# Kernel tuning notes

Measured on AMD Instinct MI355X. Metric: run time of the kernel, lower is better.

The kernel has to match this reference:

```python
import jax, jax.numpy as jnp
import numpy as np

EPS = 1e-5   # torch BatchNorm2d default eps
HEADS = 4


def conv1x1_bn(x, w, g, b, m, v):
    # 1x1 conv (no bias) == channel matmul, then inference-mode BatchNorm
    y = jnp.einsum('oc,bchw->bohw', w, x)
    s = g / jnp.sqrt(v + EPS)
    return y * s[None, :, None, None] + (b - m * s)[None, :, None, None]


def dwconv3x3_bn(x, w, g, b, m, v):
    # depthwise 3x3 conv, padding 1 (autopad), groups=C, then BatchNorm
    C = x.shape[1]
    y = jax.lax.conv_general_dilated(
        x, w, window_strides=(1, 1), padding=((1, 1), (1, 1)),
        dimension_numbers=('NCHW', 'OIHW', 'NCHW'), feature_group_count=C)
    s = g / jnp.sqrt(v + EPS)
    return y * s[None, :, None, None] + (b - m * s)[None, :, None, None]


def split_heads(x):
    b, c, h, w = x.shape
    hd = c // HEADS
    return x.reshape(b, HEADS, hd, h * w).transpose(0, 1, 3, 2)  # [b,heads,n,hd]


def merge_heads(x, h, w):
    b, heads, n, hd = x.shape
    return x.transpose(0, 1, 3, 2).reshape(b, heads * hd, h, w)


def setup_inputs() -> dict:
    key = jax.random.key(0)
    B, C, H, W = 4, 256, 48, 48
    ks = jax.random.split(key, 32)
    inp = {
        'q': jax.random.normal(ks[0], (B, C, H, W), jnp.float32),
        'k': jax.random.normal(ks[1], (B, C, H, W), jnp.float32),
        'v': jax.random.normal(ks[2], (B, C, H, W), jnp.float32),
    }
    i = 3
    for name in ['wq', 'wk', 'wv', 'proj']:
        inp[name + '_w'] = jax.random.normal(ks[i], (C, C), jnp.float32) * 0.02; i += 1
    inp['pe_w'] = jax.random.normal(ks[i], (C, 1, 3, 3), jnp.float32) * 0.1; i += 1
    for name in ['wq', 'wk', 'wv', 'pe', 'proj']:
        inp[name + '_g'] = jax.random.uniform(ks[i], (C,), jnp.float32, 0.5, 1.5); i += 1
        inp[name + '_b'] = jax.random.normal(ks[i], (C,), jnp.float32) * 0.1; i += 1
        inp[name + '_m'] = jax.random.normal(ks[i], (C,), jnp.float32) * 0.1; i += 1
        inp[name + '_v'] = jax.random.uniform(ks[i], (C,), jnp.float32, 0.5, 1.5); i += 1
    return inp


def reference(q, k, v,
              wq_w, wk_w, wv_w, proj_w, pe_w,
              wq_g, wq_b, wq_m, wq_v,
              wk_g, wk_b, wk_m, wk_v,
              wv_g, wv_b, wv_m, wv_v,
              pe_g, pe_b, pe_m, pe_v,
              proj_g, proj_b, proj_m, proj_v):
    H, W = q.shape[2], q.shape[3]
    qf = conv1x1_bn(q, wq_w, wq_g, wq_b, wq_m, wq_v)
    kf = conv1x1_bn(k, wk_w, wk_g, wk_b, wk_m, wk_v)
    vf = conv1x1_bn(v, wv_w, wv_g, wv_b, wv_m, wv_v)
    qh = split_heads(qf)  # [b,heads,n,hd]
    kh = split_heads(kf)
    vh = split_heads(vf)
    scale = qh.shape[-1] ** -0.5
    attn = jax.nn.softmax(jnp.einsum('bhnd,bhmd->bhnm', qh, kh) * scale, axis=-1)
    y = jnp.einsum('bhnm,bhmd->bhnd', attn, vh)
    y = merge_heads(y, H, W) + dwconv3x3_bn(merge_heads(qh, H, W), pe_w, pe_g, pe_b, pe_m, pe_v)
    return conv1x1_bn(y, proj_w, proj_g, proj_b, proj_m, proj_v)
```

## Files before the change

### kernel.cpp

```cpp
#include <hip/hip_runtime.h>
#include <math.h>

#define HEADS 4
#define HD    64
#define CCH   256
#define NB    4
#define HH    48
#define WW    48
#define NN    (HH*WW)
#define EPSBN 1e-5f
#define KSCL  0.18033688f
#define BCN   (NB*CCH*NN)
#define NSP   4

typedef unsigned short ushort_t;
typedef __attribute__((ext_vector_type(8))) short bfrag;
typedef __attribute__((ext_vector_type(4))) float f32x4;
typedef __attribute__((ext_vector_type(16))) float f32x16;

#define MFMA   __builtin_amdgcn_mfma_f32_16x16x32_bf16
#define MFMA32 __builtin_amdgcn_mfma_f32_32x32x16_bf16

static __device__ __forceinline__ ushort_t f2bf(float x) {
    unsigned int u = __float_as_uint(x);
    unsigned int r = (u + 0x7fffu + ((u >> 16) & 1u)) >> 16;
    return (ushort_t)r;
}
static __device__ __forceinline__ unsigned cvtpk(float lo, float hi) {
    unsigned r;
    asm("v_cvt_pk_bf16_f32 %0, %1, %2" : "=v"(r) : "v"(lo), "v"(hi));
    return r;
}
static __device__ __forceinline__ float fexp2(float x) {
    float r;
    asm("v_exp_f32 %0, %1" : "=v"(r) : "v"(x));
    return r;
}
static __device__ __forceinline__ float bflo(unsigned u) { return __uint_as_float(u << 16); }
static __device__ __forceinline__ float bfhi(unsigned u) { return __uint_as_float(u & 0xffff0000u); }

static __device__ __forceinline__ void gload16(const void* g, void* l) {
    __builtin_amdgcn_global_load_lds(
        (const __attribute__((address_space(1))) void*)g,
        (__attribute__((address_space(3))) void*)l, 16, 0, 0);
}

struct PrepWP {
    const float* W[4];
    const float* G[4]; const float* Bb[4]; const float* Mm[4]; const float* Vv[4];
    const float* pew; const float* peg; const float* peb; const float* pem; const float* pev;
    ushort_t* W4; float* bias4; ushort_t* pw2; float* pbias;
};
__global__ __launch_bounds__(256)
void prep_w(PrepWP P)
{
    const int blk = blockIdx.x, tid = threadIdx.x;
    if (blk == 128) {
        int c = tid;
        float s = P.peg[c] * rsqrtf(P.pev[c] + EPSBN);
        for (int tap = 0; tap < 9; ++tap)
            P.pw2[tap * CCH + c] = f2bf(P.pew[c * 9 + tap] * s);
        P.pbias[c] = P.peb[c] - P.pem[c] * s;
        return;
    }
    int g  = blk * 256 + tid;
    int cv = g >> 13;
    int o  = (g >> 5) & 255;
    int c8 = g & 31;
    float s  = P.G[cv][o] * rsqrtf(P.Vv[cv][o] + EPSBN);
    float s2 = (cv == 1) ? s * KSCL : s;
    const float* w = P.W[cv] + (size_t)o * CCH + c8 * 8;
    uint4 u;
    u.x = cvtpk(w[0]*s2, w[1]*s2); u.y = cvtpk(w[2]*s2, w[3]*s2);
    u.z = cvtpk(w[4]*s2, w[5]*s2); u.w = cvtpk(w[6]*s2, w[7]*s2);
    *(uint4*)&P.W4[((size_t)cv * CCH + o) * CCH + c8 * 8] = u;
    if (c8 == 0) {
        float bb = (P.Bb[cv][o] - P.Mm[cv][o] * s);
        P.bias4[cv * CCH + o] = (cv == 1) ? bb * KSCL : bb;
    }
}

template<int PROJ>
__global__ __launch_bounds__(256)
void conv_gemm(const float* __restrict__ qf, const float* __restrict__ kf,
               const float* __restrict__ vf, const ushort_t* __restrict__ T,
               const ushort_t* __restrict__ W4, const float* __restrict__ bias4,
               ushort_t* __restrict__ qnd, ushort_t* __restrict__ knd,
               ushort_t* __restrict__ vcn, float* __restrict__ outf)
{
    __shared__ ushort_t Ts[64][264];
    __shared__ ushort_t Ws[64][264];
    const int nt = blockIdx.x, ot = blockIdx.y, z = blockIdx.z;
    const int which = PROJ ? 3 : (z >> 2);
    const int b = z & 3;
    const int tid = threadIdx.x;
    const int n0 = nt * 64, o0 = ot * 64;
    const ushort_t* Wsrc = W4 + (size_t)which * CCH * CCH + (size_t)o0 * CCH;
    const float*    bias = bias4 + which * CCH;

    if (!PROJ) {
#pragma unroll
        for (int i = 0; i < 8; ++i) {
            int idx = tid + i * 256;
            int r = idx >> 5, c16 = idx & 31;
            *(uint4*)&Ws[r][c16 * 8] = *(const uint4*)&Wsrc[(size_t)r * CCH + c16 * 8];
        }
        const float* Xf = (which == 0) ? qf : (which == 1) ? kf : vf;
        const float* Xb = Xf + (size_t)b * CCH * NN + n0;
        const int n = tid & 63;
#pragma unroll
        for (int p = 0; p < 8; ++p) {
            int c0 = (tid >> 6) * 8 + p * 32;
            const float* src = Xb + (size_t)c0 * NN + n;
            float vv[8];
#pragma unroll
            for (int j = 0; j < 8; ++j) vv[j] = src[(size_t)j * NN];
            uint4 u;
            u.x = cvtpk(vv[0], vv[1]); u.y = cvtpk(vv[2], vv[3]);
            u.z = cvtpk(vv[4], vv[5]); u.w = cvtpk(vv[6], vv[7]);
            *(uint4*)&Ts[n][c0] = u;
        }
    } else {
        const ushort_t* Tsrc = T + ((size_t)b * NN + n0) * CCH;
#pragma unroll
        for (int i = 0; i < 8; ++i) {
            int idx = tid + i * 256;
            int r = idx >> 5, c16 = idx & 31;
            *(uint4*)&Ts[r][c16 * 8] = *(const uint4*)&Tsrc[(size_t)r * CCH + c16 * 8];
            *(uint4*)&Ws[r][c16 * 8] = *(const uint4*)&Wsrc[(size_t)r * CCH + c16 * 8];
        }
    }
    __syncthreads();
    const int wv = tid >> 6, lane = tid & 63, lr = lane & 15, lg = lane >> 4;
    const int qn = (wv >> 1) * 32, qo = (wv & 1) * 32;
    f32x4 acc[2][2];
#pragma unroll
    for (int i = 0; i < 2; ++i)
#pragma unroll
        for (int j = 0; j < 2; ++j) acc[i][j] = (f32x4){0.f, 0.f, 0.f, 0.f};

    if (!PROJ && (z >> 2) < 2) {
#pragma unroll
        for (int k8 = 0; k8 < 8; ++k8) {
            const int kc = k8 * 32 + lg * 8;
            bfrag ta0 = *(const bfrag*)&Ts[qn + lr][kc];
            bfrag ta1 = *(const bfrag*)&Ts[qn + 16 + lr][kc];
            bfrag wa0 = *(const bfrag*)&Ws[qo + lr][kc];
            bfrag wa1 = *(const bfrag*)&Ws[qo + 16 + lr][kc];
            acc[0][0] = MFMA(ta0, wa0, acc[0][0], 0, 0, 0);
            acc[0][1] = MFMA(ta0, wa1, acc[0][1], 0, 0, 0);
            acc[1][0] = MFMA(ta1, wa0, acc[1][0], 0, 0, 0);
            acc[1][1] = MFMA(ta1, wa1, acc[1][1], 0, 0, 0);
        }
    } else {
#pragma unroll
        for (int k8 = 0; k8 < 8; ++k8) {
            const int kc = k8 * 32 + lg * 8;
            bfrag ta0 = *(const bfrag*)&Ts[qn + lr][kc];
            bfrag ta1 = *(const bfrag*)&Ts[qn + 16 + lr][kc];
            bfrag wa0 = *(const bfrag*)&Ws[qo + lr][kc];
            bfrag wa1 = *(const bfrag*)&Ws[qo + 16 + lr][kc];
            acc[0][0] = MFMA(wa0, ta0, acc[0][0], 0, 0, 0);
            acc[0][1] = MFMA(wa0, ta1, acc[0][1], 0, 0, 0);
            acc[1][0] = MFMA(wa1, ta0, acc[1][0], 0, 0, 0);
            acc[1][1] = MFMA(wa1, ta1, acc[1][1], 0, 0, 0);
        }
    }

    __syncthreads();
    if (!PROJ && which < 2) {
        ushort_t (*Ot)[72] = (ushort_t(*)[72])Ts;
        float bv[2] = { bias[o0 + qo + lr], bias[o0 + qo + 16 + lr] };
#pragma unroll
        for (int i = 0; i < 2; ++i)
#pragma unroll
            for (int j = 0; j < 2; ++j)
#pragma unroll
                for (int r = 0; r < 4; ++r)
                    Ot[qn + i * 16 + lg * 4 + r][qo + j * 16 + lr] = f2bf(acc[i][j][r] + bv[j]);
        __syncthreads();
        ushort_t* out = (which == 0) ? qnd : knd;
        for (int idx = tid; idx < 512; idx += 256) {
            int r = idx >> 3, sg = idx & 7;
            *(uint4*)&out[(((size_t)b * HEADS + ot) * NN + n0 + r) * HD + sg * 8] =
                *(const uint4*)&Ot[r][sg * 8];
        }
    } else if (!PROJ) {
        ushort_t (*Ot)[72] = (ushort_t(*)[72])Ts;
#pragma unroll
        for (int i = 0; i < 2; ++i)
#pragma unroll
            for (int r = 0; r < 4; ++r) {
                float bv = bias[o0 + qo + i * 16 + lg * 4 + r];
#pragma unroll
                for (int j = 0; j < 2; ++j)
                    Ot[qo + i * 16 + lg * 4 + r][qn + j * 16 + lr] = f2bf(acc[i][j][r] + bv);
            }
        __syncthreads();
        for (int idx = tid; idx < 512; idx += 256) {
            int r = idx >> 3, sg = idx & 7;
            *(uint4*)&vcn[((size_t)b * CCH + o0 + r) * NN + n0 + sg * 8] =
                *(const uint4*)&Ot[r][sg * 8];
        }
    } else {
        float (*Of)[68] = (float(*)[68])Ts;
#pragma unroll
        for (int i = 0; i < 2; ++i)
#pragma unroll
            for (int r = 0; r < 4; ++r) {
                float bv = bias[o0 + qo + i * 16 + lg * 4 + r];
#pragma unroll
                for (int j = 0; j < 2; ++j)
                    Of[qo + i * 16 + lg * 4 + r][qn + j * 16 + lr] = acc[i][j][r] + bv;
            }
        __syncthreads();
        for (int idx = tid; idx < 1024; idx += 256) {
            int r = idx >> 4, c4 = idx & 15;
            *(float4*)&outf[((size_t)b * CCH + o0 + r) * NN + n0 + c4 * 4] =
                *(const float4*)&Of[r][c4 * 4];
        }
    }
}

__global__ __launch_bounds__(256, 4)
void attn_kernel(const ushort_t* __restrict__ Qnd,
                 const ushort_t* __restrict__ Knd,
                 const ushort_t* __restrict__ Vcn,
                 ushort_t* __restrict__ Op,
                 float* __restrict__ Larr)
{
    __shared__ __align__(16) char smem[32768];

    const int tid = threadIdx.x;
    const int lin0 = blockIdx.x + 18 * blockIdx.y + 288 * blockIdx.z;
    const int w    = (lin0 & 7) * 144 + (lin0 >> 3);
    const int qt = w % 18;
    const int bh = (w / 18) & 15;
    const int sp = w / 288;
    const int b = bh >> 2, h = bh & 3;
    const int lane = tid & 63, wv = tid >> 6;
    const int l31 = lane & 31, hi = lane >> 5, l7 = lane & 7;
    const int lrow = lane >> 3, lslot = (lane & 7) ^ lrow;
    const int n0 = qt * 128;
    const size_t ndb = (size_t)(b * HEADS + h) * NN * HD;
    const size_t cnb = ((size_t)b * CCH + h * HD) * NN;

    const char* kgp = (const char*)(Knd + ndb) + (size_t)(sp * 576 + wv * 16 + lrow) * 128 + lslot * 16;
    const char* vgp = (const char*)(Vcn + cnb + sp * 576) + (size_t)(wv * 16 + lrow) * (NN * 2) + lslot * 16;
    char* kls = smem + wv * 2048;
    char* vls = smem + 16384 + wv * 2048;

#define STAGE(buf, t) do { \
    const char* kp_ = kgp + (size_t)(t) * 8192; \
    const char* vp_ = vgp + (size_t)(t) * 128; \
    char* kd_ = kls + (buf) * 8192; \
    char* vd_ = vls + (buf) * 8192; \
    gload16(kp_,              kd_); \
    gload16(kp_ + 1024,       kd_ + 1024); \
    gload16(vp_,              vd_); \
    gload16(vp_ + 8 * (NN*2), vd_ + 1024); \
} while (0)

    bfrag qb[4];
    {
        const ushort_t* qbase = Qnd + ndb + (size_t)(n0 + wv * 32 + l31) * HD + hi * 8;
#pragma unroll
        for (int ds = 0; ds < 4; ++ds)
            qb[ds] = *(const bfrag*)&qbase[ds * 16];
    }

    f32x16 o[2];
#pragma unroll
    for (int db = 0; db < 2; ++db)
#pragma unroll
        for (int j = 0; j < 16; ++j) o[db][j] = 0.f;
    float lacc0 = 0.f, lacc1 = 0.f;

    STAGE(0, 0);

    for (int t = 0; t < 9; ++t) {
        const int cur = t & 1;
        if (t < 8) {
            STAGE(cur ^ 1, t + 1);
            asm volatile("s_waitcnt vmcnt(4)" ::: "memory");
        } else {
            asm volatile("s_waitcnt vmcnt(0)" ::: "memory");
        }
        __builtin_amdgcn_s_barrier();
        const char* Kb = smem + cur * 8192;
        const char* Vb = smem + 16384 + cur * 8192;

        bfrag pf[4];
#pragma unroll
        for (int kb = 0; kb < 2; ++kb) {
            f32x16 s;
#pragma unroll
            for (int j = 0; j < 16; ++j) s[j] = 0.f;
            __builtin_amdgcn_s_setprio(1);
#pragma unroll
            for (int ds = 0; ds < 4; ++ds) {
                const char* ka_p = Kb + (kb * 32 + l31) * 128 + (((2 * ds + hi) ^ l7) << 4);
                bfrag ka = *(const bfrag*)ka_p;
                s = MFMA32(ka, qb[ds], s, 0, 0, 0);
            }
            __builtin_amdgcn_s_setprio(0);
            float e[16];
#pragma unroll
            for (int j = 0; j < 16; ++j) e[j] = fexp2(s[j]);
#pragma unroll
            for (int j = 0; j < 8; ++j) { lacc0 += e[2 * j]; lacc1 += e[2 * j + 1]; }
            unsigned u[4][2];
#pragma unroll
            for (int g = 0; g < 4; ++g) {
                u[g][0] = cvtpk(e[4 * g + 0], e[4 * g + 1]);
                u[g][1] = cvtpk(e[4 * g + 2], e[4 * g + 3]);
            }
#pragma unroll
            for (int ks = 0; ks < 2; ++ks) {
                asm("v_permlane32_swap_b32 %0, %1" : "+v"(u[2*ks][0]), "+v"(u[2*ks+1][0]));
                asm("v_permlane32_swap_b32 %0, %1" : "+v"(u[2*ks][1]), "+v"(u[2*ks+1][1]));
                uint4 fw = { u[2*ks][0], u[2*ks][1], u[2*ks+1][0], u[2*ks+1][1] };
                pf[kb * 2 + ks] = *(const bfrag*)&fw;
            }
        }

        __builtin_amdgcn_s_setprio(1);
#pragma unroll
        for (int db = 0; db < 2; ++db)
#pragma unroll
            for (int ks = 0; ks < 4; ++ks) {
                const char* va_p = Vb + (db * 32 + l31) * 128 + (((2 * ks + hi) ^ l7) << 4);
                bfrag va = *(const bfrag*)va_p;
                o[db] = MFMA32(va, pf[ks], o[db], 0, 0, 0);
            }
        __builtin_amdgcn_s_setprio(0);

        __builtin_amdgcn_s_barrier();
    }
#undef STAGE

    float lacc = lacc0 + lacc1;
    lacc += __shfl_xor(lacc, 32);
    if (hi == 0)
        Larr[(size_t)(sp * 16 + bh) * NN + n0 + wv * 32 + l31] = lacc;

    unsigned (*Osb)[36] = (unsigned(*)[36])smem;
    {
        int row = wv * 32 + l31;
#pragma unroll
        for (int db = 0; db < 2; ++db)
#pragma unroll
            for (int g = 0; g < 4; ++g) {
                uint2 pk;
                pk.x = cvtpk(o[db][4 * g + 0], o[db][4 * g + 1]);
                pk.y = cvtpk(o[db][4 * g + 2], o[db][4 * g + 3]);
                *(uint2*)&Osb[row][16 * db + 4 * g + 2 * hi] = pk;
            }
    }
    __syncthreads();
    ushort_t* opb = Op + (size_t)sp * BCN + ((size_t)b * NN + n0) * CCH + h * HD;
    for (int idx = tid; idx < 1024; idx += 256) {
        int n = idx >> 3, s4 = idx & 7;
        *(uint4*)&opb[(size_t)n * CCH + s4 * 8] = *(const uint4*)&Osb[n][s4 * 4];
    }
}

__global__ __launch_bounds__(256)
void fuse_kernel(const ushort_t* __restrict__ Op, const float* __restrict__ Larr,
                 const ushort_t* __restrict__ Qnd,
                 const ushort_t* __restrict__ pw2, const float* __restrict__ pbias,
                 ushort_t* __restrict__ yt)
{
    const int tid = threadIdx.x;
    const int b  = blockIdx.x / 288;
    const int n0 = (blockIdx.x % 288) * 8;
    const int c8 = tid & 31, ns = tid >> 5;
    const int n  = n0 + ns;
    const int h  = c8 >> 3, c0 = c8 * 8;

    const ushort_t* o0p = Op + ((size_t)b * NN + n) * CCH + c0;
    float acc[8] = {0.f, 0.f, 0.f, 0.f, 0.f, 0.f, 0.f, 0.f};
#pragma unroll
    for (int s = 0; s < NSP; ++s) {
        uint4 u = *(const uint4*)&o0p[(size_t)s * BCN];
        acc[0] += bflo(u.x); acc[1] += bfhi(u.x);
        acc[2] += bflo(u.y); acc[3] += bfhi(u.y);
        acc[4] += bflo(u.z); acc[5] += bfhi(u.z);
        acc[6] += bflo(u.w); acc[7] += bfhi(u.w);
    }
    int mi = (b * HEADS + h) * NN + n;
    float ls = 0.f;
#pragma unroll
    for (int s = 0; s < NSP; ++s) ls += Larr[(size_t)s * 16 * NN + mi];
    float rinv = 1.0f / ls;
#pragma unroll
    for (int j = 0; j < 8; ++j) acc[j] *= rinv;

    const int x = n % WW, y = n / WW;
    const ushort_t* qb = Qnd + (size_t)(b * HEADS + h) * NN * HD + (c8 & 7) * 8;
#pragma unroll
    for (int ky = 0; ky < 3; ++ky) {
        int yy = y + ky - 1;
        if (yy < 0 || yy >= HH) continue;
#pragma unroll
        for (int kx = 0; kx < 3; ++kx) {
            int xx = x + kx - 1;
            if (xx < 0 || xx >= WW) continue;
            int np = yy * WW + xx;
            uint4 qv = *(const uint4*)&qb[(size_t)np * HD];
            uint4 w4 = *(const uint4*)&pw2[(ky * 3 + kx) * CCH + c0];
            acc[0] += bflo(qv.x) * bflo(w4.x); acc[1] += bfhi(qv.x) * bfhi(w4.x);
            acc[2] += bflo(qv.y) * bflo(w4.y); acc[3] += bfhi(qv.y) * bfhi(w4.y);
            acc[4] += bflo(qv.z) * bflo(w4.z); acc[5] += bfhi(qv.z) * bfhi(w4.z);
            acc[6] += bflo(qv.w) * bflo(w4.w); acc[7] += bfhi(qv.w) * bfhi(w4.w);
        }
    }
    float4 p0 = *(const float4*)&pbias[c0];
    float4 p1 = *(const float4*)&pbias[c0 + 4];
    acc[0] += p0.x; acc[1] += p0.y; acc[2] += p0.z; acc[3] += p0.w;
    acc[4] += p1.x; acc[5] += p1.y; acc[6] += p1.z; acc[7] += p1.w;
    uint4 u;
    u.x = cvtpk(acc[0], acc[1]); u.y = cvtpk(acc[2], acc[3]);
    u.z = cvtpk(acc[4], acc[5]); u.w = cvtpk(acc[6], acc[7]);
    *(uint4*)&yt[((size_t)b * NN + n) * CCH + c0] = u;
}

extern "C" void kernel_launch(void* const* d_in, const int* in_sizes, int n_in,
                              void* d_out, int out_size, void* d_ws, size_t ws_size,
                              hipStream_t stream) {
    const float* q = (const float*)d_in[0];
    const float* k = (const float*)d_in[1];
    const float* v = (const float*)d_in[2];

    char* ws = (char*)d_ws;
    ushort_t* qnd  = (ushort_t*)(ws + 0);
    ushort_t* knd  = (ushort_t*)(ws + 4718592);
    ushort_t* vcn  = (ushort_t*)(ws + 9437184);
    ushort_t* Op   = (ushort_t*)(ws + 14155776);
    ushort_t* yt   = (ushort_t*)(ws + 4718592);
    float*    Larr = (float*)   (ws + 33030144);
    ushort_t* W4   = (ushort_t*)(ws + 33619968);
    float*    bias4= (float*)   (ws + 34144256);
    ushort_t* pw2  = (ushort_t*)(ws + 34148352);
    float*    pbias= (float*)   (ws + 34152960);

    PrepWP P;
    P.W[0] = (const float*)d_in[3]; P.W[1] = (const float*)d_in[4];
    P.W[2] = (const float*)d_in[5]; P.W[3] = (const float*)d_in[6];
    P.G[0]  = (const float*)d_in[8];  P.Bb[0] = (const float*)d_in[9];
    P.Mm[0] = (const float*)d_in[10]; P.Vv[0] = (const float*)d_in[11];
    P.G[1]  = (const float*)d_in[12]; P.Bb[1] = (const float*)d_in[13];
    P.Mm[1] = (const float*)d_in[14]; P.Vv[1] = (const float*)d_in[15];
    P.G[2]  = (const float*)d_in[16]; P.Bb[2] = (const float*)d_in[17];
    P.Mm[2] = (const float*)d_in[18]; P.Vv[2] = (const float*)d_in[19];
    P.G[3]  = (const float*)d_in[24]; P.Bb[3] = (const float*)d_in[25];
    P.Mm[3] = (const float*)d_in[26]; P.Vv[3] = (const float*)d_in[27];
    P.pew = (const float*)d_in[7];
    P.peg = (const float*)d_in[20]; P.peb = (const float*)d_in[21];
    P.pem = (const float*)d_in[22]; P.pev = (const float*)d_in[23];
    P.W4 = W4; P.bias4 = bias4; P.pw2 = pw2; P.pbias = pbias;

    prep_w<<<129, 256, 0, stream>>>(P);

    conv_gemm<0><<<dim3(36, 4, 12), 256, 0, stream>>>(q, k, v, nullptr, W4, bias4,
                                                      qnd, knd, vcn, nullptr);

    attn_kernel<<<dim3(18, 16, NSP), 256, 0, stream>>>(qnd, knd, vcn, Op, Larr);

    fuse_kernel<<<1152, 256, 0, stream>>>(Op, Larr, qnd, pw2, pbias, yt);

    conv_gemm<1><<<dim3(36, 4, 4), 256, 0, stream>>>(nullptr, nullptr, nullptr, yt, W4, bias4,
                                                     nullptr, nullptr, nullptr, (float*)d_out);
}
```

Measured before the change: 76.11 us.

## Use 512-thread conv GEMM blocks and reorder attention K/V prefetch barriers

The conv GEMM kernels move from 256 to 512 threads per block, so each of the eight waves computes a 16x32 sub-tile with two MFMAs per k-step instead of four, and the load and store loops are halved. This trades per-wave work for more waves to hide global load latency. In the attention loop, the next K/V stage is now issued after a full vmcnt(0) wait and barrier, and the trailing per-iteration barrier is removed. That cuts one barrier per iteration but serializes the prefetch behind the wait, so the overlap of loading with MFMA compute is reduced.

```diff
diff --git a/kernel.cpp b/kernel.cpp
--- a/kernel.cpp
+++ b/kernel.cpp
@@ -81,7 +81,7 @@
 }
 
 template<int PROJ>
-__global__ __launch_bounds__(256)
+__global__ __launch_bounds__(512)
 void conv_gemm(const float* __restrict__ qf, const float* __restrict__ kf,
                const float* __restrict__ vf, const ushort_t* __restrict__ T,
                const ushort_t* __restrict__ W4, const float* __restrict__ bias4,
@@ -100,8 +100,8 @@
 
     if (!PROJ) {
 #pragma unroll
-        for (int i = 0; i < 8; ++i) {
-            int idx = tid + i * 256;
+        for (int i = 0; i < 4; ++i) {
+            int idx = tid + i * 512;
             int r = idx >> 5, c16 = idx & 31;
             *(uint4*)&Ws[r][c16 * 8] = *(const uint4*)&Wsrc[(size_t)r * CCH + c16 * 8];
         }
@@ -109,8 +109,8 @@
         const float* Xb = Xf + (size_t)b * CCH * NN + n0;
         const int n = tid & 63;
 #pragma unroll
-        for (int p = 0; p < 8; ++p) {
-            int c0 = (tid >> 6) * 8 + p * 32;
+        for (int p = 0; p < 4; ++p) {
+            int c0 = (tid >> 6) * 8 + p * 64;
             const float* src = Xb + (size_t)c0 * NN + n;
             float vv[8];
 #pragma unroll
@@ -123,8 +123,8 @@
     } else {
         const ushort_t* Tsrc = T + ((size_t)b * NN + n0) * CCH;
 #pragma unroll
-        for (int i = 0; i < 8; ++i) {
-            int idx = tid + i * 256;
+        for (int i = 0; i < 4; ++i) {
+            int idx = tid + i * 512;
             int r = idx >> 5, c16 = idx & 31;
             *(uint4*)&Ts[r][c16 * 8] = *(const uint4*)&Tsrc[(size_t)r * CCH + c16 * 8];
             *(uint4*)&Ws[r][c16 * 8] = *(const uint4*)&Wsrc[(size_t)r * CCH + c16 * 8];
@@ -132,38 +132,30 @@
     }
     __syncthreads();
     const int wv = tid >> 6, lane = tid & 63, lr = lane & 15, lg = lane >> 4;
-    const int qn = (wv >> 1) * 32, qo = (wv & 1) * 32;
-    f32x4 acc[2][2];
-#pragma unroll
-    for (int i = 0; i < 2; ++i)
-#pragma unroll
-        for (int j = 0; j < 2; ++j) acc[i][j] = (f32x4){0.f, 0.f, 0.f, 0.f};
+    const int qn = (wv >> 1) * 16, qo = (wv & 1) * 32;
+    f32x4 acc[2];
+    acc[0] = (f32x4){0.f, 0.f, 0.f, 0.f};
+    acc[1] = (f32x4){0.f, 0.f, 0.f, 0.f};
 
     if (!PROJ && (z >> 2) < 2) {
 #pragma unroll
         for (int k8 = 0; k8 < 8; ++k8) {
             const int kc = k8 * 32 + lg * 8;
-            bfrag ta0 = *(const bfrag*)&Ts[qn + lr][kc];
-            bfrag ta1 = *(const bfrag*)&Ts[qn + 16 + lr][kc];
+            bfrag ta  = *(const bfrag*)&Ts[qn + lr][kc];
             bfrag wa0 = *(const bfrag*)&Ws[qo + lr][kc];
             bfrag wa1 = *(const bfrag*)&Ws[qo + 16 + lr][kc];
-            acc[0][0] = MFMA(ta0, wa0, acc[0][0], 0, 0, 0);
-            acc[0][1] = MFMA(ta0, wa1, acc[0][1], 0, 0, 0);
-            acc[1][0] = MFMA(ta1, wa0, acc[1][0], 0, 0, 0);
-            acc[1][1] = MFMA(ta1, wa1, acc[1][1], 0, 0, 0);
+            acc[0] = MFMA(ta, wa0, acc[0], 0, 0, 0);
+            acc[1] = MFMA(ta, wa1, acc[1], 0, 0, 0);
         }
     } else {
 #pragma unroll
         for (int k8 = 0; k8 < 8; ++k8) {
             const int kc = k8 * 32 + lg * 8;
-            bfrag ta0 = *(const bfrag*)&Ts[qn + lr][kc];
-            bfrag ta1 = *(const bfrag*)&Ts[qn + 16 + lr][kc];
+            bfrag ta  = *(const bfrag*)&Ts[qn + lr][kc];
             bfrag wa0 = *(const bfrag*)&Ws[qo + lr][kc];
             bfrag wa1 = *(const bfrag*)&Ws[qo + 16 + lr][kc];
-            acc[0][0] = MFMA(wa0, ta0, acc[0][0], 0, 0, 0);
-            acc[0][1] = MFMA(wa0, ta1, acc[0][1], 0, 0, 0);
-            acc[1][0] = MFMA(wa1, ta0, acc[1][0], 0, 0, 0);
-            acc[1][1] = MFMA(wa1, ta1, acc[1][1], 0, 0, 0);
+            acc[0] = MFMA(wa0, ta, acc[0], 0, 0, 0);
+            acc[1] = MFMA(wa1, ta, acc[1], 0, 0, 0);
         }
     }
 
@@ -172,49 +164,45 @@
         ushort_t (*Ot)[72] = (ushort_t(*)[72])Ts;
         float bv[2] = { bias[o0 + qo + lr], bias[o0 + qo + 16 + lr] };
 #pragma unroll
-        for (int i = 0; i < 2; ++i)
-#pragma unroll
-            for (int j = 0; j < 2; ++j)
-#pragma unroll
-                for (int r = 0; r < 4; ++r)
-                    Ot[qn + i * 16 + lg * 4 + r][qo + j * 16 + lr] = f2bf(acc[i][j][r] + bv[j]);
+        for (int j = 0; j < 2; ++j)
+#pragma unroll
+            for (int r = 0; r < 4; ++r)
+                Ot[qn + lg * 4 + r][qo + j * 16 + lr] = f2bf(acc[j][r] + bv[j]);
         __syncthreads();
         ushort_t* out = (which == 0) ? qnd : knd;
-        for (int idx = tid; idx < 512; idx += 256) {
-            int r = idx >> 3, sg = idx & 7;
+        {
+            int r = tid >> 3, sg = tid & 7;
             *(uint4*)&out[(((size_t)b * HEADS + ot) * NN + n0 + r) * HD + sg * 8] =
                 *(const uint4*)&Ot[r][sg * 8];
         }
     } else if (!PROJ) {
         ushort_t (*Ot)[72] = (ushort_t(*)[72])Ts;
 #pragma unroll
-        for (int i = 0; i < 2; ++i)
+        for (int j = 0; j < 2; ++j)
 #pragma unroll
             for (int r = 0; r < 4; ++r) {
-                float bv = bias[o0 + qo + i * 16 + lg * 4 + r];
-#pragma unroll
-                for (int j = 0; j < 2; ++j)
-                    Ot[qo + i * 16 + lg * 4 + r][qn + j * 16 + lr] = f2bf(acc[i][j][r] + bv);
+                float bv = bias[o0 + qo + j * 16 + lg * 4 + r];
+                Ot[qo + j * 16 + lg * 4 + r][qn + lr] = f2bf(acc[j][r] + bv);
             }
         __syncthreads();
-        for (int idx = tid; idx < 512; idx += 256) {
-            int r = idx >> 3, sg = idx & 7;
+        {
+            int r = tid >> 3, sg = tid & 7;
             *(uint4*)&vcn[((size_t)b * CCH + o0 + r) * NN + n0 + sg * 8] =
                 *(const uint4*)&Ot[r][sg * 8];
         }
     } else {
         float (*Of)[68] = (float(*)[68])Ts;
 #pragma unroll
-        for (int i = 0; i < 2; ++i)
+        for (int j = 0; j < 2; ++j)
 #pragma unroll
             for (int r = 0; r < 4; ++r) {
-                float bv = bias[o0 + qo + i * 16 + lg * 4 + r];
-#pragma unroll
-                for (int j = 0; j < 2; ++j)
-                    Of[qo + i * 16 + lg * 4 + r][qn + j * 16 + lr] = acc[i][j][r] + bv;
+                float bv = bias[o0 + qo + j * 16 + lg * 4 + r];
+                Of[qo + j * 16 + lg * 4 + r][qn + lr] = acc[j][r] + bv;
             }
         __syncthreads();
-        for (int idx = tid; idx < 1024; idx += 256) {
+#pragma unroll
+        for (int i = 0; i < 2; ++i) {
+            int idx = tid + i * 512;
             int r = idx >> 4, c4 = idx & 15;
             *(float4*)&outf[((size_t)b * CCH + o0 + r) * NN + n0 + c4 * 4] =
                 *(const float4*)&Of[r][c4 * 4];
@@ -280,13 +268,9 @@
 
     for (int t = 0; t < 9; ++t) {
         const int cur = t & 1;
-        if (t < 8) {
-            STAGE(cur ^ 1, t + 1);
-            asm volatile("s_waitcnt vmcnt(4)" ::: "memory");
-        } else {
-            asm volatile("s_waitcnt vmcnt(0)" ::: "memory");
-        }
+        asm volatile("s_waitcnt vmcnt(0)" ::: "memory");
         __builtin_amdgcn_s_barrier();
+        if (t < 8) STAGE(cur ^ 1, t + 1);
         const char* Kb = smem + cur * 8192;
         const char* Vb = smem + 16384 + cur * 8192;
 
@@ -334,10 +318,9 @@
                 o[db] = MFMA32(va, pf[ks], o[db], 0, 0, 0);
             }
         __builtin_amdgcn_s_setprio(0);
-
-        __builtin_amdgcn_s_barrier();
     }
 #undef STAGE
+    __builtin_amdgcn_s_barrier();
 
     float lacc = lacc0 + lacc1;
     lacc += __shfl_xor(lacc, 32);
@@ -462,13 +445,13 @@
 
     prep_w<<<129, 256, 0, stream>>>(P);
 
-    conv_gemm<0><<<dim3(36, 4, 12), 256, 0, stream>>>(q, k, v, nullptr, W4, bias4,
+    conv_gemm<0><<<dim3(36, 4, 12), 512, 0, stream>>>(q, k, v, nullptr, W4, bias4,
                                                       qnd, knd, vcn, nullptr);
 
     attn_kernel<<<dim3(18, 16, NSP), 256, 0, stream>>>(qnd, knd, vcn, Op, Larr);
 
     fuse_kernel<<<1152, 256, 0, stream>>>(Op, Larr, qnd, pw2, pbias, yt);
 
-    conv_gemm<1><<<dim3(36, 4, 4), 256, 0, stream>>>(nullptr, nullptr, nullptr, yt, W4, bias4,
+    conv_gemm<1><<<dim3(36, 4, 4), 512, 0, stream>>>(nullptr, nullptr, nullptr, yt, W4, bias4,
                                                      nullptr, nullptr, nullptr, (float*)d_out);
 }
```

Result: no change. 75.10 us (-1.3%).
